# Optimization experiments

Measured on AMD Instinct MI355X. Metric: run time of the kernel, lower is better.

Reference implementation:

```python
import jax, jax.numpy as jnp
import numpy as np

# Module hyperparameters (init_kwargs)
FS = 30.0          # sampling rate (Hz)
HIGH_PASS = 40.0   # bpm
LOW_PASS = 250.0   # bpm
DELTA_T = 300      # crop length (samples)
K = 64             # crops per (batch, channel)
B, C, T = 256, 16, 9000

NBINS = DELTA_T // 2 + 1  # rfft bins
# freqs = linspace(0, Fs/2, NBINS); band mask is static given shapes
_freqs = np.linspace(0.0, FS / 2.0, NBINS)
MASK_IDX = np.where((_freqs >= HIGH_PASS / 60.0) & (_freqs <= LOW_PASS / 60.0))[0]


def setup_inputs() -> dict:
    key = jax.random.key(0)
    k1, k2 = jax.random.split(key)
    inp = jax.random.normal(k1, (B, C, T), dtype=jnp.float32)
    # random temporal offsets, one per (b, c, k) crop
    offsets = jax.random.randint(k2, (B, C, K), 0, T - DELTA_T + 1, dtype=jnp.int32)
    return {"input": inp, "offsets": offsets}


def reference(input, offsets):
    # Batched gather of all random crops: [B, C, K, DELTA_T]
    t_idx = offsets[..., None] + jnp.arange(DELTA_T, dtype=jnp.int32)  # [B,C,K,dt]
    crops = jnp.take_along_axis(input[:, :, None, :], t_idx, axis=-1)
    # Remove per-crop mean
    crops = crops - jnp.mean(crops, axis=-1, keepdims=True)
    # rFFT with 'forward' norm (divide by n), power spectrum
    spec = jnp.fft.rfft(crops, axis=-1, norm='forward')   # [B,C,K,NBINS] complex
    power = spec.real ** 2 + spec.imag ** 2               # [B,C,K,NBINS]
    # Keep only the heart-rate band (static index set), normalize to unit sum
    power = power[..., MASK_IDX]                          # [B,C,K,F_band]
    power = power / jnp.sum(power, axis=-1, keepdims=True)
    return power
```

## Files before the change

kernel.cpp:

```cpp
#include <hip/hip_runtime.h>
#include <math.h>

#define TT 9000
#define DT 300
#define KK 64
#define NB 35
#define KMIN 7
#define NCH 4096
#define NPAIR (KK * NB)


typedef __bf16 bf16;
typedef __attribute__((ext_vector_type(8))) __bf16 bf16x8;
typedef __attribute__((ext_vector_type(4))) __bf16 bf16x4;
typedef __attribute__((ext_vector_type(4))) float f32x4;

#define NFRAG_ELEMS (10 * 6 * 64 * 8)
#define WBYTES 61440

__global__ void build_w(bf16* __restrict__ tab) {
    int i = blockIdx.x * blockDim.x + threadIdx.x;
    if (i >= NFRAG_ELEMS) return;
    int j    = i & 7;
    int l    = (i >> 3) & 63;
    int f    = i >> 9;
    int nt   = f % 6;
    int ks   = f / 6;
    int quad = l >> 4;
    int c    = l & 15;
    int k    = ks * 32 + quad * 8 + j;
    int jf   = (nt % 3) * 16 + c;
    float v = 0.0f;
    if (jf <= NB - 1 && k < DT) {
        int bin = jf + KMIN;
        int ph  = (bin * k) % DT;
        float ang = 0.02094395102393195f * (float)ph;
        v = (nt >= 3) ? sinf(ang) : cosf(ang);
    }
    tab[i] = (bf16)v;
}

#define SPAD 9024
#define CPB  8
#define NBLK (NCH / CPB)

__global__ __launch_bounds__(256, 2) void st_mfma(
        const float* __restrict__ input,
        const int*   __restrict__ offsets,
        const bf16*  __restrict__ tab,
        float*       __restrict__ out) {
    __shared__ __align__(16) bf16 sig[SPAD];
    __shared__ __align__(16) unsigned char wlds[WBYTES];
    __shared__ int offs[KK];

    const int tid  = threadIdx.x;
    const int w    = tid >> 6;
    const int lane = tid & 63;
    const int quad = lane >> 4;
    const int c    = lane & 15;

#pragma unroll
    for (int i = 0; i < 15; ++i) {
        int chunk = w * 15 + i;
        __builtin_amdgcn_global_load_lds(
            (const __attribute__((address_space(1))) void*)((const unsigned char*)tab + chunk * 1024 + lane * 16),
            (__attribute__((address_space(3))) void*)(wlds + chunk * 1024),
            16, 0, 0);
    }

#pragma unroll 1
    for (int ch = 0; ch < CPB; ++ch) {
        const int chg = blockIdx.x * CPB + ch;

        const float4* src = (const float4*)(input + (size_t)chg * TT);
#pragma unroll
        for (int i = 0; i < 9; ++i) {
            int idx = tid + i * 256;
            if (idx < TT / 4) {
                float4 v = src[idx];
                bf16x4 b;
                b[0] = (bf16)v.x; b[1] = (bf16)v.y; b[2] = (bf16)v.z; b[3] = (bf16)v.w;
                *(bf16x4*)(sig + idx * 4) = b;
            }
        }
        if (tid < SPAD - TT) sig[TT + tid] = (bf16)0.0f;
        if (tid < KK) offs[tid] = offsets[(size_t)chg * KK + tid];
        __syncthreads();

        const int off = offs[w * 16 + c];
        const int d0  = (off + quad * 8) >> 1;
        const unsigned sh = (unsigned)((off & 1) << 4);
        const int* ip = (const int*)sig;

        f32x4 acc[6];
#pragma unroll
        for (int nt = 0; nt < 6; ++nt) acc[nt] = (f32x4){0.f, 0.f, 0.f, 0.f};

#pragma unroll
        for (int ks = 0; ks < 10; ++ks) {
            const int db = d0 + ks * 16;
            int dw0 = ip[db + 0], dw1 = ip[db + 1], dw2 = ip[db + 2],
                dw3 = ip[db + 3], dw4 = ip[db + 4];
            union { unsigned u[4]; bf16x8 v; } a;
            a.u[0] = __builtin_amdgcn_alignbit((unsigned)dw1, (unsigned)dw0, sh);
            a.u[1] = __builtin_amdgcn_alignbit((unsigned)dw2, (unsigned)dw1, sh);
            a.u[2] = __builtin_amdgcn_alignbit((unsigned)dw3, (unsigned)dw2, sh);
            a.u[3] = __builtin_amdgcn_alignbit((unsigned)dw4, (unsigned)dw3, sh);

#pragma unroll
            for (int nt = 0; nt < 6; ++nt) {
                bf16x8 wf = *(const bf16x8*)(wlds + ks * 6144 + nt * 1024 + lane * 16);
                acc[nt] = __builtin_amdgcn_mfma_f32_16x16x32_bf16(a.v, wf, acc[nt], 0, 0, 0);
            }
        }

        float* o = out + (size_t)chg * NPAIR;
#pragma unroll
        for (int r = 0; r < 4; ++r) {
            float p0 = acc[0][r] * acc[0][r] + acc[3][r] * acc[3][r];
            float p1 = acc[1][r] * acc[1][r] + acc[4][r] * acc[4][r];
            float p2 = acc[2][r] * acc[2][r] + acc[5][r] * acc[5][r];
            float s = p0 + p1 + ((c <= 2) ? p2 : 0.0f);
#pragma unroll
            for (int d = 1; d < 16; d <<= 1) s += __shfl_xor(s, d, 64);
            float rinv = 1.0f / s;
            int crop = w * 16 + quad * 4 + r;
            float* oc = o + crop * NB;
            oc[c] = p0 * rinv;
            oc[16 + c] = p1 * rinv;
            if (c <= 2) oc[32 + c] = p2 * rinv;
        }
        __syncthreads();
    }
}

extern "C" void kernel_launch(void* const* d_in, const int* in_sizes, int n_in,
                              void* d_out, int out_size, void* d_ws, size_t ws_size,
                              hipStream_t stream) {
    const float* input   = (const float*)d_in[0];
    const int*   offsets = (const int*)d_in[1];
    float*       out     = (float*)d_out;
    bf16*        tab     = (bf16*)d_ws;

    build_w<<<(NFRAG_ELEMS + 255) / 256, 256, 0, stream>>>(tab);
    st_mfma<<<NBLK, 256, 0, stream>>>(input, offsets, tab, out);
}
```

Baseline: 243.2 us.

## Process four channels per block iteration with register prefetch of next group

Restructures the kernel into 1024-thread blocks that hold four channel signals in LDS at once, one channel per group of four waves. The input and offsets for the next channel group are loaded into registers during the MFMA compute of the current group, then converted to bf16 and written to LDS after a barrier. This aims to hide global-load latency that was previously exposed before each channel's compute. It trades higher register pressure and a larger LDS footprint for one resident block per CU.

```diff
diff --git a/kernel.cpp b/kernel.cpp
--- a/kernel.cpp
+++ b/kernel.cpp
@@ -41,56 +41,86 @@
 }
 
 #define SPAD 9024
-#define CPB  8
+#define CHPI 4
+#define NIT  4
+#define CPB  (CHPI * NIT)
 #define NBLK (NCH / CPB)
 
-__global__ __launch_bounds__(256, 2) void st_mfma(
+__global__ __launch_bounds__(1024, 1) void st_mfma(
         const float* __restrict__ input,
         const int*   __restrict__ offsets,
         const bf16*  __restrict__ tab,
         float*       __restrict__ out) {
-    __shared__ __align__(16) bf16 sig[SPAD];
+    __shared__ __align__(16) bf16 sig[CHPI][SPAD];
     __shared__ __align__(16) unsigned char wlds[WBYTES];
-    __shared__ int offs[KK];
+    __shared__ int offs[CHPI * KK];
 
     const int tid  = threadIdx.x;
-    const int w    = tid >> 6;
+    const int wid  = tid >> 6;
     const int lane = tid & 63;
+    const int cg   = tid >> 8;
+    const int st   = tid & 255;
+    const int ch0  = blockIdx.x * CPB;
+
+    if (wid < 15) {
+#pragma unroll
+        for (int i = 0; i < 4; ++i) {
+            int chunk = wid * 4 + i;
+            __builtin_amdgcn_global_load_lds(
+                (const __attribute__((address_space(1))) void*)((const unsigned char*)tab + chunk * 1024 + lane * 16),
+                (__attribute__((address_space(3))) void*)(wlds + chunk * 1024),
+                16, 0, 0);
+        }
+    }
+    if (st < SPAD - TT) sig[cg][TT + st] = (bf16)0.0f;
+
+    float4 rb[9];
+    int roff = 0;
+    {
+        const float4* src = (const float4*)(input + (size_t)(ch0 + cg) * TT);
+#pragma unroll
+        for (int i = 0; i < 9; ++i) {
+            int idx = st + i * 256;
+            if (idx < TT / 4) rb[i] = src[idx];
+        }
+        if (tid < CHPI * KK) roff = offsets[(size_t)ch0 * KK + tid];
+    }
+#pragma unroll
+    for (int i = 0; i < 9; ++i) {
+        int idx = st + i * 256;
+        if (idx < TT / 4) {
+            bf16x4 b;
+            b[0] = (bf16)rb[i].x; b[1] = (bf16)rb[i].y;
+            b[2] = (bf16)rb[i].z; b[3] = (bf16)rb[i].w;
+            *(bf16x4*)(&sig[cg][idx * 4]) = b;
+        }
+    }
+    if (tid < CHPI * KK) offs[tid] = roff;
+    __syncthreads();
+
+    const int chl  = wid >> 2;
+    const int m    = wid & 3;
     const int quad = lane >> 4;
     const int c    = lane & 15;
 
+#pragma unroll 1
+    for (int it = 0; it < NIT; ++it) {
+        if (it + 1 < NIT) {
+            const float4* src = (const float4*)(input + (size_t)(ch0 + (it + 1) * CHPI + cg) * TT);
 #pragma unroll
-    for (int i = 0; i < 15; ++i) {
-        int chunk = w * 15 + i;
-        __builtin_amdgcn_global_load_lds(
-            (const __attribute__((address_space(1))) void*)((const unsigned char*)tab + chunk * 1024 + lane * 16),
-            (__attribute__((address_space(3))) void*)(wlds + chunk * 1024),
-            16, 0, 0);
-    }
+            for (int i = 0; i < 9; ++i) {
+                int idx = st + i * 256;
+                if (idx < TT / 4) rb[i] = src[idx];
+            }
+            if (tid < CHPI * KK)
+                roff = offsets[(size_t)(ch0 + (it + 1) * CHPI) * KK + tid];
+        }
 
-#pragma unroll 1
-    for (int ch = 0; ch < CPB; ++ch) {
-        const int chg = blockIdx.x * CPB + ch;
-
-        const float4* src = (const float4*)(input + (size_t)chg * TT);
-#pragma unroll
-        for (int i = 0; i < 9; ++i) {
-            int idx = tid + i * 256;
-            if (idx < TT / 4) {
-                float4 v = src[idx];
-                bf16x4 b;
-                b[0] = (bf16)v.x; b[1] = (bf16)v.y; b[2] = (bf16)v.z; b[3] = (bf16)v.w;
-                *(bf16x4*)(sig + idx * 4) = b;
-            }
-        }
-        if (tid < SPAD - TT) sig[TT + tid] = (bf16)0.0f;
-        if (tid < KK) offs[tid] = offsets[(size_t)chg * KK + tid];
-        __syncthreads();
-
-        const int off = offs[w * 16 + c];
+        const int chg = ch0 + it * CHPI + chl;
+        const int off = offs[chl * KK + m * 16 + c];
         const int d0  = (off + quad * 8) >> 1;
         const unsigned sh = (unsigned)((off & 1) << 4);
-        const int* ip = (const int*)sig;
+        const int* ip = (const int*)&sig[chl][0];
 
         f32x4 acc[6];
 #pragma unroll
@@ -106,7 +136,6 @@
             a.u[1] = __builtin_amdgcn_alignbit((unsigned)dw2, (unsigned)dw1, sh);
             a.u[2] = __builtin_amdgcn_alignbit((unsigned)dw3, (unsigned)dw2, sh);
             a.u[3] = __builtin_amdgcn_alignbit((unsigned)dw4, (unsigned)dw3, sh);
-
 #pragma unroll
             for (int nt = 0; nt < 6; ++nt) {
                 bf16x8 wf = *(const bf16x8*)(wlds + ks * 6144 + nt * 1024 + lane * 16);
@@ -124,13 +153,29 @@
 #pragma unroll
             for (int d = 1; d < 16; d <<= 1) s += __shfl_xor(s, d, 64);
             float rinv = 1.0f / s;
-            int crop = w * 16 + quad * 4 + r;
+            int crop = m * 16 + quad * 4 + r;
             float* oc = o + crop * NB;
             oc[c] = p0 * rinv;
             oc[16 + c] = p1 * rinv;
             if (c <= 2) oc[32 + c] = p2 * rinv;
         }
+
         __syncthreads();
+
+        if (it + 1 < NIT) {
+#pragma unroll
+            for (int i = 0; i < 9; ++i) {
+                int idx = st + i * 256;
+                if (idx < TT / 4) {
+                    bf16x4 b;
+                    b[0] = (bf16)rb[i].x; b[1] = (bf16)rb[i].y;
+                    b[2] = (bf16)rb[i].z; b[3] = (bf16)rb[i].w;
+                    *(bf16x4*)(&sig[cg][idx * 4]) = b;
+                }
+            }
+            if (tid < CHPI * KK) offs[tid] = roff;
+            __syncthreads();
+        }
     }
 }
 
@@ -143,5 +188,5 @@
     bf16*        tab     = (bf16*)d_ws;
 
     build_w<<<(NFRAG_ELEMS + 255) / 256, 256, 0, stream>>>(tab);
-    st_mfma<<<NBLK, 256, 0, stream>>>(input, offsets, tab, out);
+    st_mfma<<<NBLK, 1024, 0, stream>>>(input, offsets, tab, out);
 }
```

New measurement: 225.4 us. 7.3% less time.
